# Kernel tuning notes

Measured on AMD Instinct MI355X. Metric: run time of the kernel, lower is better.

## Reference

```python
import jax, jax.numpy as jnp
import numpy as np

V, E, H = 32000, 512, 1024
B, T = 32, 48
PAD = 0


def setup_inputs() -> dict:
    key = jax.random.key(0)
    ks = jax.random.split(key, 9)
    s = 0.05
    emb = jax.random.normal(ks[0], (V, E), jnp.float32) * s
    emb = emb.at[PAD].set(0.0)  # padding_idx row is zero in nn.Embedding
    return {
        "initial_hidden_state": jax.random.normal(ks[1], (B, H), jnp.float32),
        "target_sequence": jax.random.randint(ks[2], (B, T), 0, V),
        "emb": emb,
        "W_ih": jax.random.normal(ks[3], (3 * H, E), jnp.float32) * s,  # [r;z;n] input weights
        "W_hh": jax.random.normal(ks[4], (3 * H, H), jnp.float32) * s,
        "b_ih": jax.random.normal(ks[5], (3 * H,), jnp.float32) * s,
        "b_hh": jax.random.normal(ks[6], (3 * H,), jnp.float32) * s,
        "W_cls": jax.random.normal(ks[7], (V, H), jnp.float32) * s,
        "b_cls": jax.random.normal(ks[8], (V,), jnp.float32) * s,
    }


def _decode(initial_hidden_state, target_sequence, emb, W_ih, W_hh, b_ih, b_hh, W_cls, b_cls):
    # teacher forcing: sample_probability = 0.0 -> use_sample False
    idx_t = target_sequence.T  # [T, B]

    def step(h, y_idx):
        x = emb[y_idx]                                 # [B, E] embedding gather
        gi = x @ W_ih.T + b_ih                         # [B, 3H]
        gh = h @ W_hh.T + b_hh                         # [B, 3H]
        i_r, i_z, i_n = jnp.split(gi, 3, axis=-1)
        h_r, h_z, h_n = jnp.split(gh, 3, axis=-1)
        r = jax.nn.sigmoid(i_r + h_r)
        z = jax.nn.sigmoid(i_z + h_z)
        n = jnp.tanh(i_n + r * h_n)
        h_new = (1.0 - z) * n + z * h                  # torch GRUCell update
        score = h_new @ W_cls.T + b_cls                # [B, V]
        return h_new, score

    _, scores = jax.lax.scan(step, initial_hidden_state, idx_t)  # [T, B, V]
    return jnp.transpose(scores, (1, 0, 2))                      # [B, T, V]


def reference(initial_hidden_state, target_sequence, emb, W_ih, W_hh, b_ih, b_hh, W_cls, b_cls):
    return _decode(initial_hidden_state, target_sequence, emb, W_ih, W_hh, b_ih, b_hh, W_cls, b_cls)
```

## Files before the change

### kernel.cpp

```cpp
#include <hip/hip_runtime.h>
#include <hip/hip_bf16.h>

typedef __attribute__((ext_vector_type(8))) short short8;
typedef __attribute__((ext_vector_type(4))) float f32x4;
typedef __attribute__((ext_vector_type(4))) unsigned int u32x4;

#define T_STEPS 48
#define BATCH 32
#define EDIM 512
#define HDIM 1024
#define VOCAB 32000
#define GRU_BLOCKS 64
#define JPB 16
#define SENT 0x7FFF7FFFu
#define N_BIG 625
#define N_TILES 875
#define CNT_STRIDE 16
#define EARLY_WORKERS 96

#define HS_T_STRIDE 16384

__device__ __forceinline__ unsigned short f2bf(float f) {
    __hip_bfloat16 h = __float2bfloat16(f);
    return *reinterpret_cast<unsigned short*>(&h);
}
__device__ __forceinline__ float bf2f(unsigned short u) {
    union { unsigned int i; float f; } v;
    v.i = ((unsigned int)u) << 16;
    return v.f;
}

typedef __attribute__((address_space(1))) const void GAS;
typedef __attribute__((address_space(3))) void LAS;
__device__ __forceinline__ void gload_lds16(const unsigned short* g, unsigned short* l) {
    __builtin_amdgcn_global_load_lds((GAS*)g, (LAS*)(unsigned)(uintptr_t)l, 16, 0, 0);
}

__device__ __forceinline__ void store16_coh(unsigned int* p, u32x4 v) {
    asm volatile("global_store_dwordx4 %0, %1, off sc0 sc1"
                 :: "v"((unsigned long long)(uintptr_t)p), "v"(v) : "memory");
}

__global__ __launch_bounds__(256) void prep_kernel(
    const float* __restrict__ h0, const int* __restrict__ tseq,
    const float* __restrict__ emb, const float* __restrict__ w_ih,
    const float* __restrict__ w_hh,
    unsigned short* __restrict__ wih_bf, unsigned short* __restrict__ whh_bf,
    unsigned short* __restrict__ x_bf,
    unsigned int* __restrict__ hs32, unsigned int* __restrict__ cnt8)
{
    const long R1 = (long)3 * HDIM * EDIM / 4;
    const long R2 = (long)3 * HDIM * HDIM / 4;
    const long R3 = (long)T_STEPS * BATCH * EDIM / 4;
    const long R4 = (long)HS_T_STRIDE;
    const long R5 = (long)T_STEPS * HS_T_STRIDE / 4;
    const long R6 = 512;
    const long total = R1 + R2 + R3 + R4 + R5 + R6;

    for (long i = (long)blockIdx.x * blockDim.x + threadIdx.x; i < total;
         i += (long)gridDim.x * blockDim.x) {
        if (i < R1) {
            long j = i;
            float4 v = reinterpret_cast<const float4*>(w_ih)[j];
            ushort4 u = { f2bf(v.x), f2bf(v.y), f2bf(v.z), f2bf(v.w) };
            *reinterpret_cast<ushort4*>(wih_bf + j * 4) = u;
        } else if (i < R1 + R2) {
            long j = i - R1;
            float4 v = reinterpret_cast<const float4*>(w_hh)[j];
            ushort4 u = { f2bf(v.x), f2bf(v.y), f2bf(v.z), f2bf(v.w) };
            *reinterpret_cast<ushort4*>(whh_bf + j * 4) = u;
        } else if (i < R1 + R2 + R3) {
            long j = i - R1 - R2;
            int m = (int)(j >> 7);
            int kk4 = (int)(j & 127);
            int t = m >> 5, b = m & 31;
            int tok = tseq[b * T_STEPS + t];
            float4 v = reinterpret_cast<const float4*>(emb)[(long)tok * (EDIM / 4) + kk4];
            ushort4 u = { f2bf(v.x), f2bf(v.y), f2bf(v.z), f2bf(v.w) };
            *reinterpret_cast<ushort4*>(x_bf + (long)m * EDIM + kk4 * 4) = u;
        } else if (i < R1 + R2 + R3 + R4) {
            long j = i - R1 - R2 - R3;
            int w = (int)(j >> 5), b = (int)(j & 31);
            unsigned short a = f2bf(h0[b * HDIM + 2 * w]);
            unsigned short c = f2bf(h0[b * HDIM + 2 * w + 1]);
            hs32[j] = (unsigned)a | ((unsigned)c << 16);
        } else if (i < R1 + R2 + R3 + R4 + R5) {
            long j = i - R1 - R2 - R3 - R4;
            uint4 s = { SENT, SENT, SENT, SENT };
            reinterpret_cast<uint4*>(hs32 + HS_T_STRIDE)[j] = s;
        } else {
            long j = i - R1 - R2 - R3 - R4 - R5;
            uint4 z = { 0u, 0u, 0u, 0u };
            reinterpret_cast<uint4*>(cnt8)[j] = z;
        }
    }
}

__global__ __launch_bounds__(256) void gemm_gi(
    const unsigned short* __restrict__ A, const unsigned short* __restrict__ B,
    const float* __restrict__ bias, float* __restrict__ C, int K, int Ntot, int nM)
{
    const int nwg = gridDim.x;
    const int lin = blockIdx.x;
    const int q = nwg >> 3;
    const int wg = (lin & 7) * q + (lin >> 3);
    const int mi = wg % nM, ni = wg / nM;
    const int m0 = mi * 128, n0 = ni * 128;

    const int tid = threadIdx.x;
    const int lane = tid & 63;
    const int wid = tid >> 6;
    const int wr = wid >> 1, wc = wid & 1;

    __shared__ __align__(16) unsigned short As[128 * 32];
    __shared__ __align__(16) unsigned short Bs[128 * 32];

    f32x4 acc[4][4] = {};
    const int NT = K >> 5;
    const int srow = (lane >> 2);
    const int skk = (lane & 3) * 8;

    for (int kt = 0; kt < NT; ++kt) {
        __syncthreads();
        {
            const int kb = kt * 32;
#pragma unroll
            for (int h2 = 0; h2 < 2; ++h2) {
                const int i = wid + h2 * 4;
                const int row = i * 16 + srow;
                gload_lds16(A + (size_t)(m0 + row) * K + kb + skk, As + i * 512);
                gload_lds16(B + (size_t)(n0 + row) * K + kb + skk, Bs + i * 512);
            }
        }
        __syncthreads();

        const int kg = lane >> 4;
        const int l15 = lane & 15;
        short8 af[4], bf[4];
#pragma unroll
        for (int i = 0; i < 4; ++i) {
            af[i] = *(const short8*)(As + ((wr * 64 + i * 16 + l15) * 32 + kg * 8));
            bf[i] = *(const short8*)(Bs + ((wc * 64 + i * 16 + l15) * 32 + kg * 8));
        }
#pragma unroll
        for (int i = 0; i < 4; ++i)
#pragma unroll
            for (int j = 0; j < 4; ++j)
                acc[i][j] = __builtin_amdgcn_mfma_f32_16x16x32_bf16(af[i], bf[j], acc[i][j], 0, 0, 0);
    }

    const int l15 = lane & 15, lhi = lane >> 4;
#pragma unroll
    for (int i = 0; i < 4; ++i)
#pragma unroll
        for (int j = 0; j < 4; ++j) {
            int col = n0 + wc * 64 + j * 16 + l15;
            float bv = bias[col];
#pragma unroll
            for (int q2 = 0; q2 < 4; ++q2) {
                int row = m0 + wr * 64 + i * 16 + lhi * 4 + q2;
                C[(size_t)row * Ntot + col] = acc[i][j][q2] + bv;
            }
        }
}

__global__ __launch_bounds__(512, 1) void fused_kernel(
    unsigned int* __restrict__ hs32, unsigned int* __restrict__ hrow32,
    const unsigned short* __restrict__ whh_bf,
    const float* __restrict__ gi, const float* __restrict__ b_hh,
    const float* __restrict__ h0,
    const float* __restrict__ wcls_f, unsigned short* __restrict__ wcls_bf,
    const float* __restrict__ b_cls,
    float* __restrict__ out, unsigned int* __restrict__ cnt8,
    unsigned int* __restrict__ tileq)
{
    __shared__ __align__(16) char smem[124160];
    __shared__ unsigned short Hs[BATCH][JPB];
    __shared__ int sTile;

    const int tid = threadIdx.x;
    const int bid = blockIdx.x;
    const int lane = tid & 63, wid = tid >> 6;
    const int l15 = lane & 15, kg = lane >> 4;

    unsigned int* wcnt = cnt8 + 1056;

    if (bid < GRU_BLOCKS) {
        unsigned short (*Wl)[1032] = reinterpret_cast<unsigned short (*)[1032]>(smem);
        float (*P)[32][49] = reinterpret_cast<float (*)[32][49]>(smem + 99072);

        const int j0 = bid * JPB;
        for (int c = tid; c < 48 * 128; c += 512) {
            int row = c >> 7, k8 = (c & 127) * 8;
            int g = row >> 4, jj = row & 15;
            *(short8*)&Wl[row][k8] =
                *(const short8*)(whh_bf + (size_t)(g * HDIM + j0 + jj) * HDIM + k8);
        }
        const int b = tid >> 4, jj = tid & 15;
        const int gj = j0 + jj;
        const float bhr = b_hh[gj];
        const float bhz = b_hh[HDIM + gj];
        const float bhn = b_hh[2 * HDIM + gj];
        float hloc = h0[b * HDIM + gj];
        __syncthreads();

        for (int t = 0; t < T_STEPS; ++t) {
            const size_t tb = (size_t)t * HS_T_STRIDE;
            const float* gr = gi + (size_t)(t * BATCH + b) * (3 * HDIM);
            float xr = gr[gj], xz = gr[HDIM + gj], xn = gr[2 * HDIM + gj];

            if (tid < 256) {
                if (t) {
                    const unsigned int* cp = cnt8 + (size_t)t * CNT_STRIDE + 2 * wid;
                    for (;;) {
                        unsigned ok = (lane < 2)
                            ? (__hip_atomic_load(cp + lane, __ATOMIC_RELAXED, __HIP_MEMORY_SCOPE_AGENT) >= 8u ? 1u : 0u)
                            : 1u;
                        if (__all(ok != 0u)) break;
                        __builtin_amdgcn_s_sleep(2);
                    }
                    asm volatile("" ::: "memory");
                }

                const int kq = wid * 256;
                unsigned wv[8][8];
#pragma unroll
                for (int ks = 0; ks < 8; ++ks) {
                    const int wbase = wid * 128 + ks * 16 + kg * 4;
#pragma unroll
                    for (int mi2 = 0; mi2 < 2; ++mi2) {
                        const int bb = mi2 * 16 + l15;
#pragma unroll
                        for (int q = 0; q < 4; ++q)
                            wv[ks][mi2 * 4 + q] = *(const unsigned*)(
                                hs32 + tb + (size_t)(wbase + q) * 32 + bb);
                    }
                }
                for (;;) {
                    int bad = 0;
#pragma unroll
                    for (int ks = 0; ks < 8; ++ks)
#pragma unroll
                        for (int i = 0; i < 8; ++i)
                            bad |= (wv[ks][i] == SENT);
                    if (!__any(bad)) break;
                    __builtin_amdgcn_s_sleep(1);
#pragma unroll
                    for (int ks = 0; ks < 8; ++ks)
#pragma unroll
                        for (int i = 0; i < 8; ++i)
                            if (wv[ks][i] == SENT) {
                                const int mi2 = i >> 2, q = i & 3;
                                wv[ks][i] = __hip_atomic_load(
                                    hs32 + tb + (size_t)(wid * 128 + ks * 16 + kg * 4 + q) * 32 + (mi2 * 16 + l15),
                                    __ATOMIC_RELAXED, __HIP_MEMORY_SCOPE_AGENT);
                            }
                }
                f32x4 acc[2][3] = {};
#pragma unroll
                for (int ks = 0; ks < 8; ++ks) {
                    const int kb = kq + ks * 32 + kg * 8;
                    union U8 { unsigned u[4]; short8 s; };
                    short8 ah[2];
#pragma unroll
                    for (int mi2 = 0; mi2 < 2; ++mi2) {
                        U8 x;
#pragma unroll
                        for (int q = 0; q < 4; ++q) x.u[q] = wv[ks][mi2 * 4 + q];
                        ah[mi2] = x.s;
                    }
#pragma unroll
                    for (int fr = 0; fr < 3; ++fr) {
                        short8 bh = *(const short8*)&Wl[fr * 16 + l15][kb];
#pragma unroll
                        for (int mi2 = 0; mi2 < 2; ++mi2)
                            acc[mi2][fr] = __builtin_amdgcn_mfma_f32_16x16x32_bf16(ah[mi2], bh, acc[mi2][fr], 0, 0, 0);
                    }
                }
#pragma unroll
                for (int mi2 = 0; mi2 < 2; ++mi2)
#pragma unroll
                    for (int fr = 0; fr < 3; ++fr)
#pragma unroll
                        for (int q = 0; q < 4; ++q)
                            P[wid][mi2 * 16 + kg * 4 + q][fr * 16 + l15] = acc[mi2][fr][q];
            }
            __syncthreads();

            {
                float ghr = 0.f, ghz = 0.f, ghn = 0.f;
#pragma unroll
                for (int w = 0; w < 4; ++w) {
                    ghr += P[w][b][jj];
                    ghz += P[w][b][16 + jj];
                    ghn += P[w][b][32 + jj];
                }
                float r = 1.f / (1.f + __expf(-(xr + ghr + bhr)));
                float z = 1.f / (1.f + __expf(-(xz + ghz + bhz)));
                float n = tanhf(xn + r * (ghn + bhn));
                float hnew = (1.f - z) * n + z * hloc;
                hloc = hnew;
                Hs[b][jj] = f2bf(hnew);
            }
            __syncthreads();

            if (tid < 64) {
                const int q = tid >> 3, c = tid & 7;
                u32x4 d;
#pragma unroll
                for (int w2 = 0; w2 < 4; ++w2) {
                    int bb = c * 4 + w2;
                    d[w2] = (unsigned)Hs[bb][2 * q] | ((unsigned)Hs[bb][2 * q + 1] << 16);
                }
                store16_coh(hs32 + (size_t)(t + 1) * HS_T_STRIDE + (size_t)((j0 >> 1) + q) * 32 + c * 4, d);
            } else if (tid < 128) {
                const int i = tid - 64, bb = i >> 1, half = i & 1;
                u32x4 d;
#pragma unroll
                for (int w2 = 0; w2 < 4; ++w2) {
                    int q = half * 4 + w2;
                    d[w2] = (unsigned)Hs[bb][2 * q] | ((unsigned)Hs[bb][2 * q + 1] << 16);
                }
                store16_coh(hrow32 + ((size_t)t * BATCH + bb) * 512 + (j0 >> 1) + half * 4, d);
            }
            __syncthreads();
            if (tid == 0)
                __hip_atomic_fetch_add(cnt8 + (size_t)(t + 1) * CNT_STRIDE + (bid >> 3), 1u,
                                       __ATOMIC_RELAXED, __HIP_MEMORY_SCOPE_AGENT);
        }
    } else {
        {
            const long UNITS = (long)VOCAB * HDIM / 8;
            unsigned int* dst = (unsigned int*)wcls_bf;
            for (long u = (long)(bid - GRU_BLOCKS) * 512 + tid; u < UNITS; u += 192L * 512) {
                const float* src = wcls_f + u * 8;
                u32x4 d;
#pragma unroll
                for (int p = 0; p < 4; ++p) {
                    unsigned lo = f2bf(src[2 * p]);
                    unsigned hi = f2bf(src[2 * p + 1]);
                    d[p] = lo | (hi << 16);
                }
                store16_coh(dst + u * 4, d);
            }
            __syncthreads();
            if (tid == 0)
                __hip_atomic_fetch_add(wcnt, 1u, __ATOMIC_RELAXED, __HIP_MEMORY_SCOPE_AGENT);
        }
        if (bid >= GRU_BLOCKS + EARLY_WORKERS) {
            if (wid == 0) {
                const unsigned int* cp = cnt8 + (size_t)T_STEPS * CNT_STRIDE;
                for (;;) {
                    unsigned v = (lane < 8)
                        ? __hip_atomic_load(cp + lane, __ATOMIC_RELAXED, __HIP_MEMORY_SCOPE_AGENT)
                        : 8u;
                    if (__all(v >= 8u)) break;
                    __builtin_amdgcn_s_sleep(64);
                }
            }
            __syncthreads();
        }
    }

    if (tid == 0) {
        while (__hip_atomic_load(wcnt, __ATOMIC_RELAXED, __HIP_MEMORY_SCOPE_AGENT) < 192u)
            __builtin_amdgcn_s_sleep(16);
    }
    __syncthreads();
    asm volatile("" ::: "memory");

    const unsigned short* hrowA = (const unsigned short*)hrow32;
    const int srow = lane >> 2;
    const int skk = (lane & 3) * 8;

    for (;;) {
        __syncthreads();
        if (tid == 0)
            sTile = (int)__hip_atomic_fetch_add(tileq, 1u, __ATOMIC_RELAXED, __HIP_MEMORY_SCOPE_AGENT);
        __syncthreads();
        const int k = sTile;
        if (k >= N_TILES) break;

        int mi, m0, n0, big;
        if (k < N_BIG) { mi = k / 125; n0 = (k - mi * 125) * 256; m0 = mi * 256; big = 1; }
        else { int idx = k - N_BIG; mi = 5; m0 = 1280 + (idx & 1) * 128; n0 = (idx >> 1) * 256; big = 0; }

        {
            if (wid == 0) {
                const unsigned int* cp = cnt8 + (size_t)(mi * 8 + 8) * CNT_STRIDE;
                for (;;) {
                    unsigned v = (lane < 8)
                        ? __hip_atomic_load(cp + lane, __ATOMIC_RELAXED, __HIP_MEMORY_SCOPE_AGENT)
                        : 8u;
                    if (__all(v >= 8u)) break;
                    __builtin_amdgcn_s_sleep(32);
                }
            }
            __syncthreads();
            asm volatile("" ::: "memory");
        }

        if (big) {
            const int wm = wid >> 1, wn = wid & 1;
            unsigned short* As0 = (unsigned short*)(smem);
            unsigned short* Bs0 = (unsigned short*)(smem + 16384);
            unsigned short* As1 = (unsigned short*)(smem + 32768);
            unsigned short* Bs1 = (unsigned short*)(smem + 49152);
            f32x4 acc[4][8] = {};

#define STAGE(KT, AB, BB)                                                      \
            {                                                                  \
                const int kb = (KT) * 32;                                      \
                _Pragma("unroll")                                              \
                for (int h2 = 0; h2 < 2; ++h2) {                               \
                    const int i = wid + h2 * 8;                                \
                    const int row = i * 16 + srow;                             \
                    gload_lds16(hrowA + (size_t)(m0 + row) * HDIM + kb + skk, (AB) + i * 512); \
                    gload_lds16(wcls_bf + (size_t)(n0 + row) * HDIM + kb + skk, (BB) + i * 512); \
                }                                                              \
            }
#define COMPUTE(AB, BB)                                                        \
            {                                                                  \
                short8 af[4], bf[8];                                           \
                _Pragma("unroll")                                              \
                for (int i = 0; i < 4; ++i)                                    \
                    af[i] = *(const short8*)((AB) + ((wm * 64 + i * 16 + l15) * 32 + kg * 8)); \
                _Pragma("unroll")                                              \
                for (int j = 0; j < 8; ++j)                                    \
                    bf[j] = *(const short8*)((BB) + ((wn * 128 + j * 16 + l15) * 32 + kg * 8)); \
                _Pragma("unroll")                                              \
                for (int i = 0; i < 4; ++i)                                    \
                    _Pragma("unroll")                                          \
                    for (int j = 0; j < 8; ++j)                                \
                        acc[i][j] = __builtin_amdgcn_mfma_f32_16x16x32_bf16(af[i], bf[j], acc[i][j], 0, 0, 0); \
            }
            STAGE(0, As0, Bs0);
            __syncthreads();
            for (int it = 0; it < 16; ++it) {
                const int kt0 = 2 * it;
                STAGE(kt0 + 1, As1, Bs1);
                COMPUTE(As0, Bs0);
                __syncthreads();
                if (kt0 + 2 < 32) STAGE(kt0 + 2, As0, Bs0);
                COMPUTE(As1, Bs1);
                __syncthreads();
            }
#undef STAGE
#undef COMPUTE
            const int lhi = lane >> 4;
#pragma unroll
            for (int i = 0; i < 4; ++i)
#pragma unroll
                for (int j = 0; j < 8; ++j) {
                    int col = n0 + wn * 128 + j * 16 + l15;
                    float bv = b_cls[col];
#pragma unroll
                    for (int q2 = 0; q2 < 4; ++q2) {
                        int row = m0 + wm * 64 + i * 16 + lhi * 4 + q2;
                        int t = row >> 5, bb = row & 31;
                        __builtin_nontemporal_store(acc[i][j][q2] + bv,
                            &out[(size_t)(bb * T_STEPS + t) * VOCAB + col]);
                    }
                }
        } else {
            const int wm = wid >> 2, wn = wid & 3;
            unsigned short* As0 = (unsigned short*)(smem);
            unsigned short* Bs0 = (unsigned short*)(smem + 8192);
            unsigned short* As1 = (unsigned short*)(smem + 24576);
            unsigned short* Bs1 = (unsigned short*)(smem + 32768);
            f32x4 acc[4][4] = {};

#define STAGE1(KT, AB, BB)                                                     \
            {                                                                  \
                const int kb = (KT) * 32;                                      \
                _Pragma("unroll")                                              \
                for (int h2 = 0; h2 < 3; ++h2) {                               \
                    const int c = wid * 3 + h2;                     \
                    if (c < 8) {                                               \
                        const int row = c * 16 + srow;                         \
                        gload_lds16(hrowA + (size_t)(m0 + row) * HDIM + kb + skk, (AB) + c * 512); \
                    } else {                                                   \
                        const int row = (c - 8) * 16 + srow;                   \
                        gload_lds16(wcls_bf + (size_t)(n0 + row) * HDIM + kb + skk, (BB) + (c - 8) * 512); \
                    }                                                          \
                }                                                              \
            }
#define COMPUTE1(AB, BB)                                                       \
            {                                                                  \
                short8 af[4], bf[4];                                           \
                _Pragma("unroll")                                              \
                for (int i = 0; i < 4; ++i)                                    \
                    af[i] = *(const short8*)((AB) + ((wm * 64 + i * 16 + l15) * 32 + kg * 8)); \
                _Pragma("unroll")                                              \
                for (int j = 0; j < 4; ++j)                                    \
                    bf[j] = *(const short8*)((BB) + ((wn * 64 + j * 16 + l15) * 32 + kg * 8)); \
                _Pragma("unroll")                                              \
                for (int i = 0; i < 4; ++i)                                    \
                    _Pragma("unroll")                                          \
                    for (int j = 0; j < 4; ++j)                                \
                        acc[i][j] = __builtin_amdgcn_mfma_f32_16x16x32_bf16(af[i], bf[j], acc[i][j], 0, 0, 0); \
            }
            STAGE1(0, As0, Bs0);
            __syncthreads();
            for (int it = 0; it < 16; ++it) {
                const int kt0 = 2 * it;
                STAGE1(kt0 + 1, As1, Bs1);
                COMPUTE1(As0, Bs0);
                __syncthreads();
                if (kt0 + 2 < 32) STAGE1(kt0 + 2, As0, Bs0);
                COMPUTE1(As1, Bs1);
                __syncthreads();
            }
#undef STAGE1
#undef COMPUTE1
            const int lhi = lane >> 4;
#pragma unroll
            for (int i = 0; i < 4; ++i)
#pragma unroll
                for (int j = 0; j < 4; ++j) {
                    int col = n0 + wn * 64 + j * 16 + l15;
                    float bv = b_cls[col];
#pragma unroll
                    for (int q2 = 0; q2 < 4; ++q2) {
                        int row = m0 + wm * 64 + i * 16 + lhi * 4 + q2;
                        int t = row >> 5, bb = row & 31;
                        __builtin_nontemporal_store(acc[i][j][q2] + bv,
                            &out[(size_t)(bb * T_STEPS + t) * VOCAB + col]);
                    }
                }
        }
    }
}

extern "C" void kernel_launch(void* const* d_in, const int* in_sizes, int n_in,
                              void* d_out, int out_size, void* d_ws, size_t ws_size,
                              hipStream_t stream) {
    const float* h0    = (const float*)d_in[0];
    const int*   tseq  = (const int*)d_in[1];
    const float* emb   = (const float*)d_in[2];
    const float* w_ih  = (const float*)d_in[3];
    const float* w_hh  = (const float*)d_in[4];
    const float* b_ih  = (const float*)d_in[5];
    const float* b_hh  = (const float*)d_in[6];
    const float* w_cls = (const float*)d_in[7];
    const float* b_cls = (const float*)d_in[8];
    float* out = (float*)d_out;

    char* w = (char*)d_ws;
    unsigned short* wcls_bf = (unsigned short*)w; w += (size_t)VOCAB * HDIM * 2;
    unsigned short* wih_bf  = (unsigned short*)w; w += (size_t)3 * HDIM * EDIM * 2;
    unsigned short* whh_bf  = (unsigned short*)w; w += (size_t)3 * HDIM * HDIM * 2;
    unsigned short* x_bf    = (unsigned short*)w; w += (size_t)T_STEPS * BATCH * EDIM * 2;
    unsigned int*   hs32    = (unsigned int*)w;   w += (size_t)(T_STEPS + 1) * HS_T_STRIDE * 4;
    unsigned int*   hrow32  = (unsigned int*)w;   w += (size_t)T_STEPS * BATCH * 512 * 4;
    float* gi               = (float*)w;          w += (size_t)T_STEPS * BATCH * 3 * HDIM * 4;
    unsigned int* cnt8      = (unsigned int*)w;   w += 8192;
    unsigned int* tileq     = cnt8 + 1024;

    prep_kernel<<<2048, 256, 0, stream>>>(h0, tseq, emb, w_ih, w_hh,
                                          wih_bf, whh_bf, x_bf, hs32, cnt8);

    gemm_gi<<<(T_STEPS * BATCH / 128) * (3 * HDIM / 128), 256, 0, stream>>>(
        x_bf, wih_bf, b_ih, gi, EDIM, 3 * HDIM, T_STEPS * BATCH / 128);

    fused_kernel<<<256, 512, 0, stream>>>(hs32, hrow32, whh_bf, gi, b_hh, h0,
                                          w_cls, wcls_bf, b_cls, out, cnt8, tileq);
}
```

Before: 330.8 us.

## Fuse input-gate GEMM into persistent kernel with per-row-block readiness counters

Removes the separate gemm_gi launch and has the non-GRU worker blocks of the fused kernel compute the input-projection tiles from a dynamic tile queue before converting W_cls. Each finished tile bumps a counter for its 128-row block. GRU blocks wait for the first row block before starting and poll the counter for upcoming timesteps inside the step loop. This removes a kernel launch boundary and lets the recurrence start before the whole GEMM finishes. In exchange it adds polling in the recurrence, uses atomic scalar stores for gi, and delays the start of the W_cls conversion.

```diff
diff --git a/kernel.cpp b/kernel.cpp
--- a/kernel.cpp
+++ b/kernel.cpp
@@ -15,6 +15,7 @@
 #define SENT 0x7FFF7FFFu
 #define N_BIG 625
 #define N_TILES 875
+#define GI_TILES 288
 #define CNT_STRIDE 16
 #define EARLY_WORKERS 96
 
@@ -29,6 +30,10 @@
     v.i = ((unsigned int)u) << 16;
     return v.f;
 }
+__device__ __forceinline__ void astoref(float* p, float v) {
+    union { float f; unsigned u; } c; c.f = v;
+    __hip_atomic_store((unsigned*)p, c.u, __ATOMIC_RELAXED, __HIP_MEMORY_SCOPE_AGENT);
+}
 
 typedef __attribute__((address_space(1))) const void GAS;
 typedef __attribute__((address_space(3))) void LAS;
@@ -40,6 +45,7 @@
     asm volatile("global_store_dwordx4 %0, %1, off sc0 sc1"
                  :: "v"((unsigned long long)(uintptr_t)p), "v"(v) : "memory");
 }
+
 
 __global__ __launch_bounds__(256) void prep_kernel(
     const float* __restrict__ h0, const int* __restrict__ tseq,
@@ -96,83 +102,16 @@
     }
 }
 
-__global__ __launch_bounds__(256) void gemm_gi(
-    const unsigned short* __restrict__ A, const unsigned short* __restrict__ B,
-    const float* __restrict__ bias, float* __restrict__ C, int K, int Ntot, int nM)
-{
-    const int nwg = gridDim.x;
-    const int lin = blockIdx.x;
-    const int q = nwg >> 3;
-    const int wg = (lin & 7) * q + (lin >> 3);
-    const int mi = wg % nM, ni = wg / nM;
-    const int m0 = mi * 128, n0 = ni * 128;
-
-    const int tid = threadIdx.x;
-    const int lane = tid & 63;
-    const int wid = tid >> 6;
-    const int wr = wid >> 1, wc = wid & 1;
-
-    __shared__ __align__(16) unsigned short As[128 * 32];
-    __shared__ __align__(16) unsigned short Bs[128 * 32];
-
-    f32x4 acc[4][4] = {};
-    const int NT = K >> 5;
-    const int srow = (lane >> 2);
-    const int skk = (lane & 3) * 8;
-
-    for (int kt = 0; kt < NT; ++kt) {
-        __syncthreads();
-        {
-            const int kb = kt * 32;
-#pragma unroll
-            for (int h2 = 0; h2 < 2; ++h2) {
-                const int i = wid + h2 * 4;
-                const int row = i * 16 + srow;
-                gload_lds16(A + (size_t)(m0 + row) * K + kb + skk, As + i * 512);
-                gload_lds16(B + (size_t)(n0 + row) * K + kb + skk, Bs + i * 512);
-            }
-        }
-        __syncthreads();
-
-        const int kg = lane >> 4;
-        const int l15 = lane & 15;
-        short8 af[4], bf[4];
-#pragma unroll
-        for (int i = 0; i < 4; ++i) {
-            af[i] = *(const short8*)(As + ((wr * 64 + i * 16 + l15) * 32 + kg * 8));
-            bf[i] = *(const short8*)(Bs + ((wc * 64 + i * 16 + l15) * 32 + kg * 8));
-        }
-#pragma unroll
-        for (int i = 0; i < 4; ++i)
-#pragma unroll
-            for (int j = 0; j < 4; ++j)
-                acc[i][j] = __builtin_amdgcn_mfma_f32_16x16x32_bf16(af[i], bf[j], acc[i][j], 0, 0, 0);
-    }
-
-    const int l15 = lane & 15, lhi = lane >> 4;
-#pragma unroll
-    for (int i = 0; i < 4; ++i)
-#pragma unroll
-        for (int j = 0; j < 4; ++j) {
-            int col = n0 + wc * 64 + j * 16 + l15;
-            float bv = bias[col];
-#pragma unroll
-            for (int q2 = 0; q2 < 4; ++q2) {
-                int row = m0 + wr * 64 + i * 16 + lhi * 4 + q2;
-                C[(size_t)row * Ntot + col] = acc[i][j][q2] + bv;
-            }
-        }
-}
-
 __global__ __launch_bounds__(512, 1) void fused_kernel(
     unsigned int* __restrict__ hs32, unsigned int* __restrict__ hrow32,
     const unsigned short* __restrict__ whh_bf,
-    const float* __restrict__ gi, const float* __restrict__ b_hh,
+    float* __restrict__ gi, const float* __restrict__ b_hh,
     const float* __restrict__ h0,
     const float* __restrict__ wcls_f, unsigned short* __restrict__ wcls_bf,
     const float* __restrict__ b_cls,
-    float* __restrict__ out, unsigned int* __restrict__ cnt8,
-    unsigned int* __restrict__ tileq)
+    const unsigned short* __restrict__ x_bf, const unsigned short* __restrict__ wih_bf,
+    const float* __restrict__ b_ih,
+    float* __restrict__ out, unsigned int* __restrict__ cnt8)
 {
     __shared__ __align__(16) char smem[124160];
     __shared__ unsigned short Hs[BATCH][JPB];
@@ -183,7 +122,9 @@
     const int lane = tid & 63, wid = tid >> 6;
     const int l15 = lane & 15, kg = lane >> 4;
 
-    unsigned int* wcnt = cnt8 + 1056;
+    unsigned int* tileq   = cnt8 + 1024;
+    unsigned int* giTileq = cnt8 + 1040;
+    unsigned int* wcnt    = cnt8 + 1056;
 
     if (bid < GRU_BLOCKS) {
         unsigned short (*Wl)[1032] = reinterpret_cast<unsigned short (*)[1032]>(smem);
@@ -202,7 +143,12 @@
         const float bhz = b_hh[HDIM + gj];
         const float bhn = b_hh[2 * HDIM + gj];
         float hloc = h0[b * HDIM + gj];
+        if (tid == 0) {
+            while (__hip_atomic_load(cnt8 + 1280, __ATOMIC_RELAXED, __HIP_MEMORY_SCOPE_AGENT) < 24u)
+                __builtin_amdgcn_s_sleep(8);
+        }
         __syncthreads();
+        asm volatile("" ::: "memory");
 
         for (int t = 0; t < T_STEPS; ++t) {
             const size_t tb = (size_t)t * HS_T_STRIDE;
@@ -212,10 +158,16 @@
             if (tid < 256) {
                 if (t) {
                     const unsigned int* cp = cnt8 + (size_t)t * CNT_STRIDE + 2 * wid;
+                    const int s1 = ((t + 1) >> 2) < 12 ? ((t + 1) >> 2) : 11;
+                    const unsigned int* gq = cnt8 + 1280 + (size_t)s1 * CNT_STRIDE;
                     for (;;) {
-                        unsigned ok = (lane < 2)
-                            ? (__hip_atomic_load(cp + lane, __ATOMIC_RELAXED, __HIP_MEMORY_SCOPE_AGENT) >= 8u ? 1u : 0u)
-                            : 1u;
+                        unsigned ok;
+                        if (lane < 2)
+                            ok = (__hip_atomic_load(cp + lane, __ATOMIC_RELAXED, __HIP_MEMORY_SCOPE_AGENT) >= 8u) ? 1u : 0u;
+                        else if (lane == 2)
+                            ok = (__hip_atomic_load(gq, __ATOMIC_RELAXED, __HIP_MEMORY_SCOPE_AGENT) >= 24u) ? 1u : 0u;
+                        else
+                            ok = 1u;
                         if (__all(ok != 0u)) break;
                         __builtin_amdgcn_s_sleep(2);
                     }
@@ -329,6 +281,64 @@
                                        __ATOMIC_RELAXED, __HIP_MEMORY_SCOPE_AGENT);
         }
     } else {
+        {
+            unsigned short* As0 = (unsigned short*)(smem);
+            unsigned short* Bs0 = (unsigned short*)(smem + 8192);
+            const int srow = lane >> 2, skk = (lane & 3) * 8;
+            const int wr2 = wid >> 2, wc2 = wid & 3;
+            const int lhi = lane >> 4;
+
+            for (;;) {
+                __syncthreads();
+                if (tid == 0)
+                    sTile = (int)__hip_atomic_fetch_add(giTileq, 1u, __ATOMIC_RELAXED, __HIP_MEMORY_SCOPE_AGENT);
+                __syncthreads();
+                const int k = sTile;
+                if (k >= GI_TILES) break;
+                const int mi = k / 24, ni = k - mi * 24;
+                const int m0 = mi * 128, n0 = ni * 128;
+
+                f32x4 acc[4][2] = {};
+                for (int kt = 0; kt < 16; ++kt) {
+                    __syncthreads();
+                    {
+                        const int kb = kt * 32;
+                        const int row = wid * 16 + srow;
+                        gload_lds16(x_bf + (size_t)(m0 + row) * EDIM + kb + skk, As0 + wid * 512);
+                        gload_lds16(wih_bf + (size_t)(n0 + row) * EDIM + kb + skk, Bs0 + wid * 512);
+                    }
+                    __syncthreads();
+                    short8 af[4], bfr[2];
+#pragma unroll
+                    for (int i = 0; i < 4; ++i)
+                        af[i] = *(const short8*)(As0 + ((wr2 * 64 + i * 16 + l15) * 32 + kg * 8));
+#pragma unroll
+                    for (int j = 0; j < 2; ++j)
+                        bfr[j] = *(const short8*)(Bs0 + ((wc2 * 32 + j * 16 + l15) * 32 + kg * 8));
+#pragma unroll
+                    for (int i = 0; i < 4; ++i)
+#pragma unroll
+                        for (int j = 0; j < 2; ++j)
+                            acc[i][j] = __builtin_amdgcn_mfma_f32_16x16x32_bf16(af[i], bfr[j], acc[i][j], 0, 0, 0);
+                }
+#pragma unroll
+                for (int i = 0; i < 4; ++i)
+#pragma unroll
+                    for (int j = 0; j < 2; ++j) {
+                        int col = n0 + wc2 * 32 + j * 16 + l15;
+                        float bv = b_ih[col];
+#pragma unroll
+                        for (int q2 = 0; q2 < 4; ++q2) {
+                            int row = m0 + wr2 * 64 + i * 16 + lhi * 4 + q2;
+                            astoref(&gi[(size_t)row * (3 * HDIM) + col], acc[i][j][q2] + bv);
+                        }
+                    }
+                __syncthreads();
+                if (tid == 0)
+                    __hip_atomic_fetch_add(cnt8 + 1280 + (size_t)mi * CNT_STRIDE, 1u,
+                                           __ATOMIC_RELAXED, __HIP_MEMORY_SCOPE_AGENT);
+            }
+        }
         {
             const long UNITS = (long)VOCAB * HDIM / 8;
             unsigned int* dst = (unsigned int*)wcls_bf;
@@ -555,14 +565,11 @@
     unsigned int*   hrow32  = (unsigned int*)w;   w += (size_t)T_STEPS * BATCH * 512 * 4;
     float* gi               = (float*)w;          w += (size_t)T_STEPS * BATCH * 3 * HDIM * 4;
     unsigned int* cnt8      = (unsigned int*)w;   w += 8192;
-    unsigned int* tileq     = cnt8 + 1024;
 
     prep_kernel<<<2048, 256, 0, stream>>>(h0, tseq, emb, w_ih, w_hh,
                                           wih_bf, whh_bf, x_bf, hs32, cnt8);
 
-    gemm_gi<<<(T_STEPS * BATCH / 128) * (3 * HDIM / 128), 256, 0, stream>>>(
-        x_bf, wih_bf, b_ih, gi, EDIM, 3 * HDIM, T_STEPS * BATCH / 128);
-
     fused_kernel<<<256, 512, 0, stream>>>(hs32, hrow32, whh_bf, gi, b_hh, h0,
-                                          w_cls, wcls_bf, b_cls, out, cnt8, tileq);
-}
+                                          w_cls, wcls_bf, b_cls,
+                                          x_bf, wih_bf, b_ih, out, cnt8);
+}
```

Measured after the change: 324.4 us. Within noise of the previous version (-1.9%).
